# Kernel optimization log

Hardware: AMD Instinct MI355X
Metric: run time of the kernel (lower is better)

The kernel has to match this reference:

```python
import jax, jax.numpy as jnp
import numpy as np

IN_C = 256
OUT_C = 256
QK_C = OUT_C // 8  # channel_reduction_rate = 8
B, H, W = 8, 64, 64


def setup_inputs() -> dict:
    key = jax.random.key(0)
    ks = jax.random.split(key, 7)
    s_in = 1.0 / np.sqrt(IN_C)  # torch Conv2d default init scale (kernel=1)
    return {
        "x": jax.random.normal(ks[0], (B, IN_C, H, W), dtype=jnp.float32),
        "W1": jax.random.uniform(ks[1], (OUT_C, IN_C), jnp.float32, -s_in, s_in),
        "b1": jax.random.uniform(ks[2], (OUT_C,), jnp.float32, -s_in, s_in),
        "W2": jax.random.uniform(ks[3], (QK_C, IN_C), jnp.float32, -s_in, s_in),
        "b2": jax.random.uniform(ks[4], (QK_C,), jnp.float32, -s_in, s_in),
        "W3": jax.random.uniform(ks[5], (QK_C, IN_C), jnp.float32, -s_in, s_in),
        "b3": jax.random.uniform(ks[6], (QK_C,), jnp.float32, -s_in, s_in),
    }


def reference(x, W1, b1, W2, b2, W3, b3):
    b, c, h, w = x.shape
    n = h * w
    xf = x.reshape(b, c, n)  # 1x1 conv == channel matmul on flattened spatial
    v = jnp.einsum("oc,bcn->bon", W1, xf) + b1[None, :, None]   # [B, OUT_C, N]
    q = jnp.einsum("oc,bcn->bon", W2, xf) + b2[None, :, None]   # [B, QK_C, N]
    k = jnp.einsum("oc,bcn->bon", W3, xf) + b3[None, :, None]   # [B, QK_C, N]
    scores = jnp.einsum("bdn,bdm->bnm", q, k)                    # [B, N, N]
    # GLOBAL softmax over the full flattened NxN matrix per batch element
    attn = jax.nn.softmax(scores.reshape(b, -1), axis=1).reshape(b, n, n)
    out = jnp.einsum("bon,bnm->bom", v, attn)                    # [B, OUT_C, N]
    return out.reshape(x.shape) + x
```

## Files before the change

### kernel.cpp

```cpp
#include <hip/hip_runtime.h>
#include <hip/hip_bf16.h>
#include <math.h>

#define NBATCH 8
#define NC 256
#define ND 32
#define SN 4096

constexpr size_t VB_B   = 0;
constexpr size_t QT_B   = 16777216;
constexpr size_t KT_B   = QT_B + 2097152;
constexpr size_t PM_B   = KT_B + 2097152;
constexpr size_t PS_B   = PM_B + 32768;
constexpr size_t C_B    = PS_B + 32768;
constexpr size_t WB_B   = C_B + 64;
constexpr size_t BIAS_B = WB_B + 163840;

typedef __attribute__((ext_vector_type(8))) short short8;
typedef __attribute__((ext_vector_type(4))) float f32x4;

__device__ __forceinline__ unsigned bf16rne(float f) {
  unsigned u = __float_as_uint(f);
  return (u + 0x7fffu + ((u >> 16) & 1u)) >> 16;
}
__device__ __forceinline__ unsigned bfpack2(float lo, float hi) {
  union { __hip_bfloat162 h; unsigned u; } cv;
  cv.h.x = __float2bfloat16(lo);
  cv.h.y = __float2bfloat16(hi);
  return cv.u;
}

__global__ __launch_bounds__(256) void prep_kernel(
    const float* __restrict__ W1, const float* __restrict__ b1,
    const float* __restrict__ W2, const float* __restrict__ b2,
    const float* __restrict__ W3, const float* __restrict__ b3,
    char* __restrict__ wsb)
{
  ushort* Wb = (ushort*)(wsb + WB_B);
  float* bias = (float*)(wsb + BIAS_B);
  const float LOG2E = 1.4426950408889634f;
  int idx = blockIdx.x * 256 + threadIdx.x;
  int r = idx >> 6, c4 = (idx & 63) * 4;
  float4 v; float sc = 1.0f;
  if (r < 256)      { v = *(const float4*)(W1 + (size_t)r * 256 + c4); }
  else if (r < 288) { v = *(const float4*)(W2 + (size_t)(r - 256) * 256 + c4); sc = LOG2E; }
  else              { v = *(const float4*)(W3 + (size_t)(r - 288) * 256 + c4); }
  ushort4 o;
  o.x = (ushort)bf16rne(v.x * sc); o.y = (ushort)bf16rne(v.y * sc);
  o.z = (ushort)bf16rne(v.z * sc); o.w = (ushort)bf16rne(v.w * sc);
  *(ushort4*)(Wb + (size_t)r * 256 + c4) = o;
  if (blockIdx.x == 0 && threadIdx.x < 320) {
    int q = threadIdx.x;
    bias[q] = q < 256 ? b1[q] : (q < 288 ? b2[q - 256] * LOG2E : b3[q - 288]);
  }
}

__global__ __launch_bounds__(512) void proj_kernel(
    const float* __restrict__ x, char* __restrict__ wsb)
{
  __shared__ alignas(16) char xT[65536];
  __shared__ alignas(16) char Wsh[40960];
  const int bid = blockIdx.x;
  const int b = bid & 7, nt = bid >> 3;
  const int n0 = nt * 128;
  const int t = threadIdx.x, w = t >> 6, lane = t & 63;
  const int l4 = lane >> 4, l16 = lane & 15;
  const float* xb = x + (size_t)b * NC * SN;
  const ushort* Wb = (const ushort*)(wsb + WB_B);
  const float* bias = (const float*)(wsb + BIAS_B);
  ushort* vbuf  = (ushort*)(wsb + VB_B);
  ushort* qtbuf = (ushort*)(wsb + QT_B);
  ushort* ktbuf = (ushort*)(wsb + KT_B);

  {
    int cp = w * 16 + l16;
    int c  = cp * 2;
    int nb0 = l4 * 4;
#pragma unroll
    for (int ni = 0; ni < 8; ++ni) {
      int nB = ni * 16 + nb0;
      float4 a0 = *(const float4*)(xb + (size_t)c * SN + n0 + nB);
      float4 a1 = *(const float4*)(xb + (size_t)(c + 1) * SN + n0 + nB);
      const float* p0 = (const float*)&a0;
      const float* p1 = (const float*)&a1;
#pragma unroll
      for (int j = 0; j < 4; ++j) {
        int n = nB + j;
        *(uint*)(xT + n * 512 + ((cp * 4) ^ ((n & 7) << 4))) = bfpack2(p0[j], p1[j]);
      }
    }
  }
#pragma unroll
  for (int ii = 0; ii < 5; ++ii) {
    int slot = t + ii * 512;
    int r = slot >> 3, cc = slot & 7;
    *(uint4*)(Wsh + r * 128 + ((cc * 16) ^ ((r & 7) << 4))) =
        *(const uint4*)(Wb + (size_t)r * 256 + cc * 8);
  }
  __syncthreads();

  const int of_g = w >> 1;
  const int nf_g = w & 1;
  f32x4 acc[5][4] = {};

  for (int c4 = 0; c4 < 4; ++c4) {
#pragma unroll
    for (int kk = 0; kk < 2; ++kk) {
      short8 a[4];
#pragma unroll
      for (int nf = 0; nf < 4; ++nf) {
        int n = nf_g * 64 + nf * 16 + l16;
        a[nf] = *(const short8*)(xT + n * 512 +
                 ((c4 * 128 + kk * 64 + l4 * 16) ^ ((n & 7) << 4)));
      }
#pragma unroll
      for (int of = 0; of < 5; ++of) {
        int o = (of_g * 5 + of) * 16 + l16;
        short8 bf = *(const short8*)(Wsh + o * 128 +
                    ((kk * 64 + l4 * 16) ^ ((o & 7) << 4)));
#pragma unroll
        for (int nf = 0; nf < 4; ++nf)
          acc[of][nf] = __builtin_amdgcn_mfma_f32_16x16x32_bf16(a[nf], bf, acc[of][nf], 0, 0, 0);
      }
    }
    if (c4 < 3) {
      __syncthreads();
#pragma unroll
      for (int ii = 0; ii < 5; ++ii) {
        int slot = t + ii * 512;
        int r = slot >> 3, cc = slot & 7;
        *(uint4*)(Wsh + r * 128 + ((cc * 16) ^ ((r & 7) << 4))) =
            *(const uint4*)(Wb + (size_t)r * 256 + (c4 + 1) * 64 + cc * 8);
      }
      __syncthreads();
    }
  }

#pragma unroll
  for (int of = 0; of < 5; ++of) {
    int o = (of_g * 5 + of) * 16 + l16;
    float bv = bias[o];
#pragma unroll
    for (int nf = 0; nf < 4; ++nf) {
      int nb = nf_g * 64 + nf * 16 + l4 * 4;
      float v0 = acc[of][nf][0] + bv, v1 = acc[of][nf][1] + bv;
      float v2 = acc[of][nf][2] + bv, v3 = acc[of][nf][3] + bv;
      if (o < 256) {
        uint2 pk; pk.x = bfpack2(v0, v1); pk.y = bfpack2(v2, v3);
        *(uint2*)(vbuf + ((size_t)b * NC + o) * SN + n0 + nb) = pk;
      } else if (o < 288) {
        int d = o - 256;
        qtbuf[((size_t)b * SN + n0 + nb + 0) * ND + d] = (ushort)bf16rne(v0);
        qtbuf[((size_t)b * SN + n0 + nb + 1) * ND + d] = (ushort)bf16rne(v1);
        qtbuf[((size_t)b * SN + n0 + nb + 2) * ND + d] = (ushort)bf16rne(v2);
        qtbuf[((size_t)b * SN + n0 + nb + 3) * ND + d] = (ushort)bf16rne(v3);
      } else {
        int d = o - 288;
        ktbuf[((size_t)b * SN + n0 + nb + 0) * ND + d] = (ushort)bf16rne(v0);
        ktbuf[((size_t)b * SN + n0 + nb + 1) * ND + d] = (ushort)bf16rne(v1);
        ktbuf[((size_t)b * SN + n0 + nb + 2) * ND + d] = (ushort)bf16rne(v2);
        ktbuf[((size_t)b * SN + n0 + nb + 3) * ND + d] = (ushort)bf16rne(v3);
      }
    }
  }
}

__global__ __launch_bounds__(256) void qk_stats(
    const char* __restrict__ wsb, float* __restrict__ pm, float* __restrict__ ps)
{
  __shared__ alignas(16) char qt_s[128 * 64];
  __shared__ alignas(16) char kt_s[128 * 64];
  __shared__ float wm[4], wz[4];
  const int bid = blockIdx.x;
  const int b = bid & 7, ny = (bid >> 3) & 31, mx = bid >> 8;
  const int n0 = ny * 128, m0 = mx * 128;
  const int t = threadIdx.x, w = t >> 6, lane = t & 63;
  const int l4 = lane >> 4, l16 = lane & 15;
  const ushort* qtb = (const ushort*)(wsb + QT_B) + (size_t)b * SN * ND;
  const ushort* ktb = (const ushort*)(wsb + KT_B) + (size_t)b * SN * ND;
  {
    int row = t >> 1, db = (t & 1) * 32;
#pragma unroll
    for (int i = 0; i < 2; ++i) {
      int b16 = db + i * 16;
      int dst = row * 64 + (b16 ^ ((row & 3) << 4));
      *(uint4*)(qt_s + dst) = *(const uint4*)(qtb + (size_t)(n0 + row) * ND + b16 / 2);
      *(uint4*)(kt_s + dst) = *(const uint4*)(ktb + (size_t)(m0 + row) * ND + b16 / 2);
    }
  }
  __syncthreads();
  const f32x4 zf = {0.f, 0.f, 0.f, 0.f};
  short8 bfr[2];
#pragma unroll
  for (int j = 0; j < 2; ++j) {
    int mm = (w * 2 + j) * 16 + l16;
    bfr[j] = *(const short8*)(kt_s + mm * 64 + ((l4 * 16) ^ ((mm & 3) << 4)));
  }
  f32x4 sfr[8][2];
#pragma unroll
  for (int i = 0; i < 8; ++i) {
    int nn = i * 16 + l16;
    short8 af = *(const short8*)(qt_s + nn * 64 + ((l4 * 16) ^ ((nn & 3) << 4)));
#pragma unroll
    for (int j = 0; j < 2; ++j)
      sfr[i][j] = __builtin_amdgcn_mfma_f32_16x16x32_bf16(af, bfr[j], zf, 0, 0, 0);
  }
  float mt = -1e30f;
#pragma unroll
  for (int i = 0; i < 8; ++i)
#pragma unroll
    for (int j = 0; j < 2; ++j)
#pragma unroll
      for (int r = 0; r < 4; ++r) mt = fmaxf(mt, sfr[i][j][r]);
  float zt = 0.f;
#pragma unroll
  for (int i = 0; i < 8; ++i)
#pragma unroll
    for (int j = 0; j < 2; ++j)
#pragma unroll
      for (int r = 0; r < 4; ++r) zt += exp2f(sfr[i][j][r] - mt);

#pragma unroll
  for (int off = 1; off < 64; off <<= 1) {
    float m2 = __shfl_xor(mt, off);
    float z2 = __shfl_xor(zt, off);
    float M = fmaxf(mt, m2);
    zt = zt * exp2f(mt - M) + z2 * exp2f(m2 - M);
    mt = M;
  }
  if (lane == 0) { wm[w] = mt; wz[w] = zt; }
  __syncthreads();
  if (t == 0) {
    float m = wm[0], z = wz[0];
#pragma unroll
    for (int i = 1; i < 4; ++i) {
      float M = fmaxf(m, wm[i]);
      z = z * exp2f(m - M) + wz[i] * exp2f(wm[i] - M);
      m = M;
    }
    int idx = (b * 32 + ny) * 32 + mx;
    pm[idx] = m; ps[idx] = z;
  }
}

__global__ __launch_bounds__(256) void reduce_kernel(char* __restrict__ wsb)
{
  const int b = blockIdx.x;
  const float* pm = (const float*)(wsb + PM_B) + (size_t)b * 1024;
  const float* ps = (const float*)(wsb + PS_B) + (size_t)b * 1024;
  const int t = threadIdx.x;
  float m = -1e30f, z = 0.f;
  for (int i = t; i < 1024; i += 256) {
    float m2 = pm[i], z2 = ps[i];
    float M = fmaxf(m, m2);
    z = z * exp2f(m - M) + z2 * exp2f(m2 - M);
    m = M;
  }
#pragma unroll
  for (int off = 1; off < 64; off <<= 1) {
    float m2 = __shfl_xor(m, off);
    float z2 = __shfl_xor(z, off);
    float M = fmaxf(m, m2);
    z = z * exp2f(m - M) + z2 * exp2f(m2 - M);
    m = M;
  }
  __shared__ float wm[4], wz[4];
  int w = t >> 6;
  if ((t & 63) == 0) { wm[w] = m; wz[w] = z; }
  __syncthreads();
  if (t == 0) {
    float M = wm[0], Z = wz[0];
#pragma unroll
    for (int i = 1; i < 4; ++i) {
      float Mn = fmaxf(M, wm[i]);
      Z = Z * exp2f(M - Mn) + wz[i] * exp2f(wm[i] - Mn);
      M = Mn;
    }
    ((float*)(wsb + C_B))[b] = M + log2f(Z);
  }
}

__global__ __launch_bounds__(256) void attn_out(
    const char* __restrict__ wsb, const float* __restrict__ x, float* __restrict__ out)
{
  __shared__ alignas(16) char qt_s[2][4096];
  __shared__ alignas(16) char as_s[2][8192];
  const int bid = blockIdx.x;
  const int b = bid & 7;
  const int rest = bid >> 3;
  const int mt = rest & 63;
  const int oh = rest >> 6;
  const int m0 = mt * 64;
  const int o0 = oh * 128;
  const int t = threadIdx.x, w = t >> 6, lane = t & 63;
  const int l4 = lane >> 4, l16 = lane & 15;
  const ushort* vb  = (const ushort*)(wsb + VB_B) + (size_t)b * NC * SN;
  const ushort* qtb = (const ushort*)(wsb + QT_B) + (size_t)b * SN * ND;
  const ushort* ktb = (const ushort*)(wsb + KT_B) + (size_t)b * SN * ND;
  const float Cb = ((const float*)(wsb + C_B))[b];

  const int mS_l = w * 16 + l16;
  short8 bfr = *(const short8*)(ktb + (size_t)(m0 + mS_l) * ND + l4 * 8);

  const int as_wb = w * 1024 + l16 * 16 + (l4 & 1) * 8;
  const int l4h = l4 >> 1;

  const int qrow = t >> 2, qsl = t & 3;
  const int qt_addr = (qrow >> 4) * 1024 + ((qsl * 16 + (qrow & 15)) << 4);

  const ushort* vrow0 = vb + (size_t)(o0 + w * 32 + l16) * SN + l4 * 8;
  const ushort* vrow1 = vrow0 + (size_t)16 * SN;

  const f32x4 zf = {0.f, 0.f, 0.f, 0.f};
  f32x4 acc[2][4] = {};

  *(uint4*)(qt_s[0] + qt_addr) = *(const uint4*)(qtb + (size_t)qrow * ND + qsl * 8);
  __syncthreads();

  for (int i = 0; i < 64; ++i) {
    const int cur = i & 1;
    short8 vf[2][2];
#pragma unroll
    for (int kk = 0; kk < 2; ++kk) {
      vf[0][kk] = *(const short8*)(vrow0 + i * 64 + kk * 32);
      vf[1][kk] = *(const short8*)(vrow1 + i * 64 + kk * 32);
    }
    uint4 qnext;
    const bool pf = (i < 63);
    if (pf) qnext = *(const uint4*)(qtb + (size_t)((i + 1) * 64 + qrow) * ND + qsl * 8);

#pragma unroll
    for (int nf = 0; nf < 4; ++nf) {
      short8 af = *(const short8*)(qt_s[cur] + nf * 1024 + lane * 16);
      f32x4 sv = __builtin_amdgcn_mfma_f32_16x16x32_bf16(af, bfr, zf, 0, 0, 0);
      uint2 pk;
      pk.x = bfpack2(exp2f(sv[0] - Cb), exp2f(sv[1] - Cb));
      pk.y = bfpack2(exp2f(sv[2] - Cb), exp2f(sv[3] - Cb));
      int addr = (nf >> 1) * 4096 + (((nf & 1) * 2 + l4h) & 3) * 256 + as_wb;
      *(uint2*)(as_s[cur] + addr) = pk;
    }
    if (pf)
      *(uint4*)(qt_s[cur ^ 1] + qt_addr) = qnext;
    __syncthreads();

    __builtin_amdgcn_s_setprio(1);
#pragma unroll
    for (int kk = 0; kk < 2; ++kk) {
#pragma unroll
      for (int mf = 0; mf < 4; ++mf) {
        short8 paf = *(const short8*)(as_s[cur] + (kk * 4 + mf) * 1024 + lane * 16);
        acc[0][mf] = __builtin_amdgcn_mfma_f32_16x16x32_bf16(vf[0][kk], paf, acc[0][mf], 0, 0, 0);
        acc[1][mf] = __builtin_amdgcn_mfma_f32_16x16x32_bf16(vf[1][kk], paf, acc[1][mf], 0, 0, 0);
      }
    }
    __builtin_amdgcn_s_setprio(0);
  }

#pragma unroll
  for (int of = 0; of < 2; ++of)
#pragma unroll
    for (int mf = 0; mf < 4; ++mf) {
      int m = m0 + mf * 16 + l16;
#pragma unroll
      for (int j = 0; j < 4; ++j) {
        int o = o0 + w * 32 + of * 16 + l4 * 4 + j;
        size_t idx = ((size_t)b * NC + o) * SN + m;
        out[idx] = acc[of][mf][j] + x[idx];
      }
    }
}

extern "C" void kernel_launch(void* const* d_in, const int* in_sizes, int n_in,
                              void* d_out, int out_size, void* d_ws, size_t ws_size,
                              hipStream_t stream)
{
  const float* x  = (const float*)d_in[0];
  const float* W1 = (const float*)d_in[1];
  const float* b1 = (const float*)d_in[2];
  const float* W2 = (const float*)d_in[3];
  const float* b2 = (const float*)d_in[4];
  const float* W3 = (const float*)d_in[5];
  const float* b3 = (const float*)d_in[6];
  char* wsb  = (char*)d_ws;
  float* out = (float*)d_out;

  prep_kernel<<<80, 256, 0, stream>>>(W1, b1, W2, b2, W3, b3, wsb);
  proj_kernel<<<256, 512, 0, stream>>>(x, wsb);
  qk_stats<<<8192, 256, 0, stream>>>(wsb, (float*)(wsb + PM_B), (float*)(wsb + PS_B));
  reduce_kernel<<<NBATCH, 256, 0, stream>>>(wsb);
  attn_out<<<1024, 256, 0, stream>>>(wsb, x, out);
}
```

Measured before the change: 211.8 us.

## Restructure attn_out so each wave owns all output channels for its columns

The attention-output kernel is retiled: each 512-thread block covers 128 m-columns, and each wave handles 16 columns across all 256 output channels with 16 accumulators. The exp(QK) tile is computed once per wave instead of being recomputed for each output-channel half, and is kept in a per-wave LDS slice. Q is read straight from global memory rather than staged in shared memory. The softmax offset is folded into the MFMA accumulator init. In exchange, V fragments are now loaded directly from global memory, 16 per k-step per wave, and register pressure is higher with only 256 blocks launched.

Result: slower. 656.5 us (+209.9%).

```diff
diff --git a/kernel.cpp b/kernel.cpp
--- a/kernel.cpp
+++ b/kernel.cpp
@@ -280,18 +280,12 @@
   }
 }
 
-__global__ __launch_bounds__(256) void attn_out(
+__global__ __launch_bounds__(512) void attn_out(
     const char* __restrict__ wsb, const float* __restrict__ x, float* __restrict__ out)
 {
-  __shared__ alignas(16) char qt_s[2][4096];
-  __shared__ alignas(16) char as_s[2][8192];
+  __shared__ alignas(16) char p_s[16384];
   const int bid = blockIdx.x;
-  const int b = bid & 7;
-  const int rest = bid >> 3;
-  const int mt = rest & 63;
-  const int oh = rest >> 6;
-  const int m0 = mt * 64;
-  const int o0 = oh * 128;
+  const int b = bid & 7, mt = bid >> 3;
   const int t = threadIdx.x, w = t >> 6, lane = t & 63;
   const int l4 = lane >> 4, l16 = lane & 15;
   const ushort* vb  = (const ushort*)(wsb + VB_B) + (size_t)b * NC * SN;
@@ -299,75 +293,55 @@
   const ushort* ktb = (const ushort*)(wsb + KT_B) + (size_t)b * SN * ND;
   const float Cb = ((const float*)(wsb + C_B))[b];
 
-  const int mS_l = w * 16 + l16;
-  short8 bfr = *(const short8*)(ktb + (size_t)(m0 + mS_l) * ND + l4 * 8);
-
-  const int as_wb = w * 1024 + l16 * 16 + (l4 & 1) * 8;
+  const int m0 = mt * 128 + w * 16;
+  short8 bfr = *(const short8*)(ktb + (size_t)(m0 + l16) * ND + l4 * 8);
+  const f32x4 cinit = {-Cb, -Cb, -Cb, -Cb};
+
+  char* myp = p_s + w * 2048;
+  const int pw_base = l16 * 16 + (l4 & 1) * 8;
   const int l4h = l4 >> 1;
 
-  const int qrow = t >> 2, qsl = t & 3;
-  const int qt_addr = (qrow >> 4) * 1024 + ((qsl * 16 + (qrow & 15)) << 4);
-
-  const ushort* vrow0 = vb + (size_t)(o0 + w * 32 + l16) * SN + l4 * 8;
-  const ushort* vrow1 = vrow0 + (size_t)16 * SN;
-
-  const f32x4 zf = {0.f, 0.f, 0.f, 0.f};
-  f32x4 acc[2][4] = {};
-
-  *(uint4*)(qt_s[0] + qt_addr) = *(const uint4*)(qtb + (size_t)qrow * ND + qsl * 8);
-  __syncthreads();
+  const ushort* vrow = vb + (size_t)l16 * SN + l4 * 8;
+
+  f32x4 acc[16];
+#pragma unroll
+  for (int of = 0; of < 16; ++of) acc[of] = (f32x4){0.f, 0.f, 0.f, 0.f};
 
   for (int i = 0; i < 64; ++i) {
-    const int cur = i & 1;
-    short8 vf[2][2];
+    const int n0 = i * 64;
+#pragma unroll
+    for (int nf = 0; nf < 4; ++nf) {
+      short8 af = *(const short8*)(qtb + (size_t)(n0 + nf * 16 + l16) * ND + l4 * 8);
+      f32x4 sv = __builtin_amdgcn_mfma_f32_16x16x32_bf16(af, bfr, cinit, 0, 0, 0);
+      uint2 pk;
+      pk.x = bfpack2(exp2f(sv[0]), exp2f(sv[1]));
+      pk.y = bfpack2(exp2f(sv[2]), exp2f(sv[3]));
+      *(uint2*)(myp + (nf >> 1) * 1024 + (2 * (nf & 1) + l4h) * 256 + pw_base) = pk;
+    }
+    __builtin_amdgcn_s_setprio(1);
 #pragma unroll
     for (int kk = 0; kk < 2; ++kk) {
-      vf[0][kk] = *(const short8*)(vrow0 + i * 64 + kk * 32);
-      vf[1][kk] = *(const short8*)(vrow1 + i * 64 + kk * 32);
-    }
-    uint4 qnext;
-    const bool pf = (i < 63);
-    if (pf) qnext = *(const uint4*)(qtb + (size_t)((i + 1) * 64 + qrow) * ND + qsl * 8);
-
-#pragma unroll
-    for (int nf = 0; nf < 4; ++nf) {
-      short8 af = *(const short8*)(qt_s[cur] + nf * 1024 + lane * 16);
-      f32x4 sv = __builtin_amdgcn_mfma_f32_16x16x32_bf16(af, bfr, zf, 0, 0, 0);
-      uint2 pk;
-      pk.x = bfpack2(exp2f(sv[0] - Cb), exp2f(sv[1] - Cb));
-      pk.y = bfpack2(exp2f(sv[2] - Cb), exp2f(sv[3] - Cb));
-      int addr = (nf >> 1) * 4096 + (((nf & 1) * 2 + l4h) & 3) * 256 + as_wb;
-      *(uint2*)(as_s[cur] + addr) = pk;
-    }
-    if (pf)
-      *(uint4*)(qt_s[cur ^ 1] + qt_addr) = qnext;
+      short8 paf = *(const short8*)(myp + kk * 1024 + lane * 16);
+      const ushort* vkk = vrow + n0 + kk * 32;
+#pragma unroll
+      for (int of = 0; of < 16; ++of) {
+        short8 vf = *(const short8*)(vkk + (size_t)(of * 16) * SN);
+        acc[of] = __builtin_amdgcn_mfma_f32_16x16x32_bf16(vf, paf, acc[of], 0, 0, 0);
+      }
+    }
+    __builtin_amdgcn_s_setprio(0);
     __syncthreads();
-
-    __builtin_amdgcn_s_setprio(1);
-#pragma unroll
-    for (int kk = 0; kk < 2; ++kk) {
-#pragma unroll
-      for (int mf = 0; mf < 4; ++mf) {
-        short8 paf = *(const short8*)(as_s[cur] + (kk * 4 + mf) * 1024 + lane * 16);
-        acc[0][mf] = __builtin_amdgcn_mfma_f32_16x16x32_bf16(vf[0][kk], paf, acc[0][mf], 0, 0, 0);
-        acc[1][mf] = __builtin_amdgcn_mfma_f32_16x16x32_bf16(vf[1][kk], paf, acc[1][mf], 0, 0, 0);
-      }
-    }
-    __builtin_amdgcn_s_setprio(0);
-  }
-
-#pragma unroll
-  for (int of = 0; of < 2; ++of)
-#pragma unroll
-    for (int mf = 0; mf < 4; ++mf) {
-      int m = m0 + mf * 16 + l16;
-#pragma unroll
-      for (int j = 0; j < 4; ++j) {
-        int o = o0 + w * 32 + of * 16 + l4 * 4 + j;
-        size_t idx = ((size_t)b * NC + o) * SN + m;
-        out[idx] = acc[of][mf][j] + x[idx];
-      }
-    }
+  }
+
+#pragma unroll
+  for (int of = 0; of < 16; ++of) {
+#pragma unroll
+    for (int j = 0; j < 4; ++j) {
+      int o = of * 16 + l4 * 4 + j;
+      size_t idx = ((size_t)b * NC + o) * SN + m0 + l16;
+      out[idx] = acc[of][j] + x[idx];
+    }
+  }
 }
 
 extern "C" void kernel_launch(void* const* d_in, const int* in_sizes, int n_in,
@@ -388,5 +362,5 @@
   proj_kernel<<<256, 512, 0, stream>>>(x, wsb);
   qk_stats<<<8192, 256, 0, stream>>>(wsb, (float*)(wsb + PM_B), (float*)(wsb + PS_B));
   reduce_kernel<<<NBATCH, 256, 0, stream>>>(wsb);
-  attn_out<<<1024, 256, 0, stream>>>(wsb, x, out);
-}
+  attn_out<<<256, 512, 0, stream>>>(wsb, x, out);
+}
```
